# Performance work log

Hardware: AMD Instinct MI355X
Metric: run time of the kernel (lower is better)

## Reference

```python
import jax, jax.numpy as jnp
import numpy as np

B, H, W, C = 1, 64, 64, 256
HEADS, K, DIL = 8, 7, 2
HD = C // HEADS
FF = 4 * C
EPS = 1e-5
SCALE = 1.0 / float(np.sqrt(HD))


def _axis_indices(L, k, d):
    """NATTEN dilated neighborhood: per dilation-group clamped sliding window.
    Returns key indices [L,k] and relative-position-bias indices [L,k]."""
    i = np.arange(L)
    g, rem = i // d, i % d                      # position within dilation group
    lg = (L - rem + d - 1) // d                 # group length per position
    start = np.clip(g - k // 2, 0, lg - k)      # clamped window start (group coords)
    a = np.arange(k)
    kidx = (start[:, None] + a[None, :]) * d + rem[:, None]          # key coord
    bidx = start[:, None] + a[None, :] - g[:, None] + (k - 1)        # rpb coord in [0, 2k-2]
    return kidx.astype(np.int32), bidx.astype(np.int32)


def setup_inputs():
    key = jax.random.key(0)
    ks = jax.random.split(key, 8)
    p = lambda k_, sh: jax.random.normal(k_, sh, jnp.float32) * 0.02
    return {
        "x": jax.random.normal(ks[0], (B, H, W, C), jnp.float32),
        "ln1_g": jnp.ones((C,), jnp.float32), "ln1_b": jnp.zeros((C,), jnp.float32),
        "wq": p(ks[1], (C, C)), "bq": jnp.zeros((C,), jnp.float32),
        "wk": p(ks[2], (C, C)), "bk": jnp.zeros((C,), jnp.float32),
        "wv": p(ks[3], (C, C)), "bv": jnp.zeros((C,), jnp.float32),
        "rpb": p(ks[4], (HEADS, 2 * K - 1, 2 * K - 1)),
        "wo": p(ks[5], (C, C)), "bo": jnp.zeros((C,), jnp.float32),
        "ln2_g": jnp.ones((C,), jnp.float32), "ln2_b": jnp.zeros((C,), jnp.float32),
        "w1": p(ks[6], (C, FF)), "b1": jnp.zeros((FF,), jnp.float32),
        "w2": p(ks[7], (FF, C)), "b2": jnp.zeros((C,), jnp.float32),
    }


def _layer_norm(x, g, b):
    m = jnp.mean(x, -1, keepdims=True)
    v = jnp.mean(jnp.square(x - m), -1, keepdims=True)
    return (x - m) * jax.lax.rsqrt(v + EPS) * g + b


def reference(x, ln1_g, ln1_b, wq, bq, wk, bk, wv, bv, rpb, wo, bo,
              ln2_g, ln2_b, w1, b1, w2, b2):
    ih, bih = _axis_indices(H, K, DIL)   # [H,K]
    iw, biw = _axis_indices(W, K, DIL)   # [W,K]
    hs = _layer_norm(x, ln1_g, ln1_b)
    q = (hs @ wq + bq).reshape(B, H, W, HEADS, HD) * SCALE
    k = (hs @ wk + bk).reshape(B, H, W, HEADS, HD)
    v = (hs @ wv + bv).reshape(B, H, W, HEADS, HD)
    # gather dilated neighborhoods -> [B,H,W,K,K,heads,hd]
    k_nb = k[:, ih[:, None, :, None], iw[None, :, None, :], :, :]
    v_nb = v[:, ih[:, None, :, None], iw[None, :, None, :], :, :]
    # natten2dqkrpb: per-query scores over K*K dilated neighbors + rpb
    scores = jnp.einsum('bijnc,bijklnc->bnijkl', q, k_nb)
    bias = rpb[:, bih[:, None, :, None], biw[None, :, None, :]]  # [heads,H,W,K,K]
    scores = scores + bias[None]
    probs = jax.nn.softmax(scores.reshape(B, HEADS, H, W, K * K), axis=-1)
    # natten2dav
    ctx = jnp.einsum('bnijp,bijpnc->bijnc', probs,
                     v_nb.reshape(B, H, W, K * K, HEADS, HD))
    attn_out = ctx.reshape(B, H, W, C) @ wo + bo
    hs2 = x + attn_out                      # residual (layer_scale disabled: init 0.0)
    y = _layer_norm(hs2, ln2_g, ln2_b)
    y = jax.nn.gelu(y @ w1 + b1, approximate=False) @ w2 + b2
    return hs2 + y
```

## Files before the change

kernel.cpp:

```cpp
#include <hip/hip_runtime.h>
#include <math.h>

#define CC 256
#define NTOK 4096
#define NHEADS 8
#define HD 32
#define FFD 1024
#define LN_EPS 1e-5f
#define QSCALE 0.17677669529663687f

typedef __bf16 bf16x8 __attribute__((ext_vector_type(8)));
typedef float f32x4 __attribute__((ext_vector_type(4)));
typedef unsigned short u16x8 __attribute__((ext_vector_type(8)));

__device__ __forceinline__ unsigned short f2bf(float f) {
    unsigned u = __builtin_bit_cast(unsigned, f);
    u += 0x7fff + ((u >> 16) & 1);
    return (unsigned short)(u >> 16);
}
__device__ __forceinline__ float bf2f(unsigned short h) {
    unsigned u = ((unsigned)h) << 16;
    return __builtin_bit_cast(float, u);
}
__device__ __forceinline__ void gload16(const unsigned short* g, unsigned short* l) {
    __builtin_amdgcn_global_load_lds(
        (const __attribute__((address_space(1))) unsigned int*)(const void*)g,
        (__attribute__((address_space(3))) unsigned int*)(void*)l, 16, 0, 0);
}

__global__ void ln_kernel(const float* __restrict__ x, const float* __restrict__ g,
                          const float* __restrict__ b, unsigned short* __restrict__ out) {
    int wave = threadIdx.x >> 6;
    int lane = threadIdx.x & 63;
    int tok = blockIdx.x * 4 + wave;
    const float4 v = ((const float4*)(x + (size_t)tok * CC))[lane];
    float s  = v.x + v.y + v.z + v.w;
    float ss = v.x * v.x + v.y * v.y + v.z * v.z + v.w * v.w;
    #pragma unroll
    for (int o = 32; o > 0; o >>= 1) { s += __shfl_xor(s, o); ss += __shfl_xor(ss, o); }
    float m   = s * (1.0f / CC);
    float var = ss * (1.0f / CC) - m * m;
    float r   = rsqrtf(var + LN_EPS);
    float4 gv = ((const float4*)g)[lane];
    float4 bv = ((const float4*)b)[lane];
    ushort4 o4;
    o4.x = f2bf((v.x - m) * r * gv.x + bv.x);
    o4.y = f2bf((v.y - m) * r * gv.y + bv.y);
    o4.z = f2bf((v.z - m) * r * gv.z + bv.z);
    o4.w = f2bf((v.w - m) * r * gv.w + bv.w);
    ((ushort4*)(out + (size_t)tok * CC))[lane] = o4;
}

__global__ void setup_kernel(const float* __restrict__ wq, const float* __restrict__ wk,
                             const float* __restrict__ wv, const float* __restrict__ wo,
                             const float* __restrict__ w1, const float* __restrict__ w2,
                             const float* __restrict__ bq, const float* __restrict__ bk,
                             const float* __restrict__ bv,
                             unsigned short* __restrict__ wt_qkv, unsigned short* __restrict__ wo_t,
                             unsigned short* __restrict__ w1_t, unsigned short* __restrict__ w2_t,
                             float* __restrict__ bqkv) {
    int id = blockIdx.x;
    int t = threadIdx.x;
    if (id == 192) {
        bqkv[t]       = bq[t] * QSCALE;
        bqkv[256 + t] = bk[t];
        bqkv[512 + t] = bv[t];
        return;
    }
    const float* src; unsigned short* dst;
    int Kd, N, rowoff = 0, bx, by; float scale = 1.0f;
    if (id < 16)       { src = wq; dst = wt_qkv; Kd = 256;  N = 256;  scale = QSCALE; int l = id;       bx = l & 3;  by = l >> 2; }
    else if (id < 32)  { src = wk; dst = wt_qkv; Kd = 256;  N = 256;  rowoff = 256;   int l = id - 16;  bx = l & 3;  by = l >> 2; }
    else if (id < 48)  { src = wv; dst = wt_qkv; Kd = 256;  N = 256;  rowoff = 512;   int l = id - 32;  bx = l & 3;  by = l >> 2; }
    else if (id < 64)  { src = wo; dst = wo_t;   Kd = 256;  N = 256;                  int l = id - 48;  bx = l & 3;  by = l >> 2; }
    else if (id < 128) { src = w1; dst = w1_t;   Kd = 256;  N = 1024;                 int l = id - 64;  bx = l & 15; by = l >> 4; }
    else               { src = w2; dst = w2_t;   Kd = 1024; N = 256;                  int l = id - 128; bx = l & 3;  by = l >> 2; }
    int n0 = bx * 64, k0 = by * 64;
    __shared__ float tile[64][65];
    int cc = t & 63, rb = t >> 6;
    #pragma unroll
    for (int i = 0; i < 16; i++) {
        int r = rb + i * 4;
        tile[r][cc] = src[(size_t)(k0 + r) * N + n0 + cc];
    }
    __syncthreads();
    int n = t >> 2;
    #pragma unroll
    for (int i = 0; i < 8; i++) {
        int p = (t & 3) + i * 4;
        unsigned lo = f2bf(tile[2 * p][n] * scale);
        unsigned hi = f2bf(tile[2 * p + 1][n] * scale);
        *(unsigned*)(dst + (size_t)(rowoff + n0 + n) * Kd + k0 + 2 * p) = lo | (hi << 16);
    }
}

template<int BM, int BN, int KD, int ACT, bool ADD_RES, bool OUT_BF16>
__global__ __launch_bounds__(256) void mfma_gemm(
    const unsigned short* __restrict__ A, const unsigned short* __restrict__ Bt,
    const float* __restrict__ bias, const float* __restrict__ res,
    void* __restrict__ Cm, int N) {
    constexpr int WM = BM / 2, WN = BN / 2;
    constexpr int MF = WM / 16, NF = WN / 16;
    constexpr int NIT = KD / 32;
    __shared__ unsigned short lds[2][(BM + BN) * 32];
    const int t = threadIdx.x;
    const int lane = t & 63, w = t >> 6;
    const int wr = w >> 1, wc = w & 1;
    const int bm = blockIdx.y * BM, bn = blockIdx.x * BN;
    const int fr = lane & 15, sq = lane >> 4;
    const int aoff = (wr * WM + fr) * 64 + sq * 16;
    const int boff = (wc * WN + fr) * 64 + sq * 16;

    auto stage = [&](int it, int buf) {
        unsigned short* La = lds[buf];
        unsigned short* Lb = lds[buf] + BM * 32;
        if (BM * 4 == 256 || t < BM * 4)
            gload16(A + (size_t)(bm + (t >> 2)) * KD + it * 32 + (t & 3) * 8, La + t * 8);
        gload16(Bt + (size_t)(bn + (t >> 2)) * KD + it * 32 + (t & 3) * 8, Lb + t * 8);
    };

    f32x4 acc[MF][NF] = {};
    stage(0, 0);
    #pragma unroll
    for (int it = 0; it < NIT; ++it) {
        const int buf = it & 1;
        __syncthreads();
        if (it + 1 < NIT) stage(it + 1, buf ^ 1);
        const char* La = (const char*)lds[buf];
        const char* Lb = (const char*)(lds[buf] + BM * 32);
        bf16x8 af[MF], bfr[NF];
        #pragma unroll
        for (int i = 0; i < MF; i++) af[i] = *(const bf16x8*)(La + aoff + i * 1024);
        #pragma unroll
        for (int j = 0; j < NF; j++) bfr[j] = *(const bf16x8*)(Lb + boff + j * 1024);
        #pragma unroll
        for (int i = 0; i < MF; i++)
            #pragma unroll
            for (int j = 0; j < NF; j++)
                acc[i][j] = __builtin_amdgcn_mfma_f32_16x16x32_bf16(af[i], bfr[j], acc[i][j], 0, 0, 0);
    }
    #pragma unroll
    for (int i = 0; i < MF; i++) {
        int row0 = bm + wr * WM + i * 16 + sq * 4;
        #pragma unroll
        for (int j = 0; j < NF; j++) {
            int col = bn + wc * WN + j * 16 + fr;
            float bvv = bias[col];
            #pragma unroll
            for (int r = 0; r < 4; r++) {
                float v = acc[i][j][r] + bvv;
                if constexpr (ACT == 1) v = 0.5f * v * (1.0f + erff(v * 0.70710678118654752f));
                if constexpr (ADD_RES) v += res[(size_t)(row0 + r) * N + col];
                if constexpr (OUT_BF16)
                    ((unsigned short*)Cm)[(size_t)(row0 + r) * N + col] = f2bf(v);
                else
                    ((float*)Cm)[(size_t)(row0 + r) * N + col] = v;
            }
        }
    }
}

__global__ void attn_kernel(const unsigned short* __restrict__ qkv,
                            const float* __restrict__ rpb,
                            unsigned short* __restrict__ ctx) {
    __shared__ float ps[4][64];
    int wave = threadIdx.x >> 6;
    int lane = threadIdx.x & 63;
    int gid  = blockIdx.x * 4 + wave;
    int tok  = gid >> 3;
    int head = gid & 7;
    int i = tok >> 6, j = tok & 63;
    int gi = i >> 1, ri = i & 1;
    int gj = j >> 1, rj = j & 1;
    int si = min(max(gi - 3, 0), 25);
    int sj = min(max(gj - 3, 0), 25);

    float score = -1e30f;
    if (lane < 49) {
        int a1 = lane / 7, a2 = lane % 7;
        int kt = ((si + a1) * 2 + ri) * 64 + (sj + a2) * 2 + rj;
        const unsigned short* qp = qkv + (size_t)tok * 768 + head * HD;
        const unsigned short* kp = qkv + (size_t)kt * 768 + 256 + head * HD;
        float s = 0.0f;
        #pragma unroll
        for (int d = 0; d < HD; d += 8) {
            u16x8 qv8 = *(const u16x8*)(qp + d);
            u16x8 kv8 = *(const u16x8*)(kp + d);
            #pragma unroll
            for (int e = 0; e < 8; e++) s += bf2f(qv8[e]) * bf2f(kv8[e]);
        }
        score = s + rpb[(head * 13 + (si + a1 - gi + 6)) * 13 + (sj + a2 - gj + 6)];
    }
    float mx = score;
    #pragma unroll
    for (int o = 32; o > 0; o >>= 1) mx = fmaxf(mx, __shfl_xor(mx, o));
    float p = (lane < 49) ? __expf(score - mx) : 0.0f;
    float sum = p;
    #pragma unroll
    for (int o = 32; o > 0; o >>= 1) sum += __shfl_xor(sum, o);
    ps[wave][lane] = p / sum;

    int d = lane & 31, half = lane >> 5;
    const unsigned short* vb = qkv + 512 + head * HD + d;
    float acc = 0.0f;
    #pragma unroll
    for (int s = 0; s < 25; ++s) {
        int nb = 2 * s + half;
        if (nb < 49) {
            int a1 = nb / 7, a2 = nb % 7;
            int kt = ((si + a1) * 2 + ri) * 64 + (sj + a2) * 2 + rj;
            acc += ps[wave][nb] * bf2f(vb[(size_t)kt * 768]);
        }
    }
    acc += __shfl_xor(acc, 32);
    if (lane < HD)
        ctx[(size_t)tok * CC + head * HD + lane] = f2bf(acc);
}

extern "C" void kernel_launch(void* const* d_in, const int* in_sizes, int n_in,
                              void* d_out, int out_size, void* d_ws, size_t ws_size,
                              hipStream_t stream) {
    const float* x     = (const float*)d_in[0];
    const float* ln1_g = (const float*)d_in[1];
    const float* ln1_b = (const float*)d_in[2];
    const float* wq    = (const float*)d_in[3];
    const float* bq    = (const float*)d_in[4];
    const float* wk    = (const float*)d_in[5];
    const float* bk    = (const float*)d_in[6];
    const float* wv    = (const float*)d_in[7];
    const float* bv    = (const float*)d_in[8];
    const float* rpb   = (const float*)d_in[9];
    const float* wo    = (const float*)d_in[10];
    const float* bo    = (const float*)d_in[11];
    const float* ln2_g = (const float*)d_in[12];
    const float* ln2_b = (const float*)d_in[13];
    const float* w1    = (const float*)d_in[14];
    const float* b1    = (const float*)d_in[15];
    const float* w2    = (const float*)d_in[16];
    const float* b2    = (const float*)d_in[17];

    char* wsb = (char*)d_ws;
    unsigned short* hs_bf  = (unsigned short*)(wsb);
    unsigned short* qkv_bf = (unsigned short*)(wsb + (2u << 20));
    unsigned short* ctx_bf = (unsigned short*)(wsb + (8u << 20));
    float*          hs2    = (float*)(wsb + (10u << 20));
    unsigned short* y1_bf  = (unsigned short*)(wsb + (14u << 20));
    unsigned short* gm_bf  = (unsigned short*)(wsb + (16u << 20));
    unsigned short* wt_qkv = (unsigned short*)(wsb + (24u << 20));
    unsigned short* wo_t   = wt_qkv + 768 * 256;
    unsigned short* w1_t   = wo_t + 256 * 256;
    unsigned short* w2_t   = w1_t + 1024 * 256;
    float*          bqkv   = (float*)(w2_t + 256 * 1024);

    setup_kernel<<<193, 256, 0, stream>>>(wq, wk, wv, wo, w1, w2, bq, bk, bv,
                                          wt_qkv, wo_t, w1_t, w2_t, bqkv);
    ln_kernel<<<NTOK / 4, 256, 0, stream>>>(x, ln1_g, ln1_b, hs_bf);
    mfma_gemm<64, 64, 256, 0, false, true><<<dim3(12, 64), 256, 0, stream>>>(
        hs_bf, wt_qkv, bqkv, nullptr, qkv_bf, 768);
    attn_kernel<<<NTOK * NHEADS / 4, 256, 0, stream>>>(qkv_bf, rpb, ctx_bf);
    mfma_gemm<32, 64, 256, 0, true, false><<<dim3(4, 128), 256, 0, stream>>>(
        ctx_bf, wo_t, bo, x, hs2, 256);
    ln_kernel<<<NTOK / 4, 256, 0, stream>>>(hs2, ln2_g, ln2_b, y1_bf);
    mfma_gemm<64, 64, 256, 1, false, true><<<dim3(16, 64), 256, 0, stream>>>(
        y1_bf, w1_t, b1, nullptr, gm_bf, 1024);
    mfma_gemm<32, 64, 1024, 0, true, false><<<dim3(4, 128), 256, 0, stream>>>(
        gm_bf, w2_t, b2, hs2, (float*)d_out, 256);
}
```

Before: 164.7 us.

## Load full K into LDS for K=256 GEMMs, deepen pipeline stages, restructure attention per token

The K=256 GEMMs now load the whole A and B K-slab into LDS with a single barrier instead of a double-buffered loop of 32-wide steps. The K=1024 GEMM now uses 64-wide double-buffered stages, which halves the number of barriers. The attention kernel now runs one wave per token covering all 8 heads, with 8 lanes per head. Each lane handles 4 channels and reduces with shuffles, so the query and neighbour K/V rows are read as contiguous 512-byte segments instead of many scattered per-lane loads. Full-K staging uses more LDS per block (up to 64 KB), which may lower occupancy.

```diff
diff --git a/kernel.cpp b/kernel.cpp
--- a/kernel.cpp
+++ b/kernel.cpp
@@ -11,7 +11,6 @@
 
 typedef __bf16 bf16x8 __attribute__((ext_vector_type(8)));
 typedef float f32x4 __attribute__((ext_vector_type(4)));
-typedef unsigned short u16x8 __attribute__((ext_vector_type(8)));
 
 __device__ __forceinline__ unsigned short f2bf(float f) {
     unsigned u = __builtin_bit_cast(unsigned, f);
@@ -94,45 +93,48 @@
     }
 }
 
-template<int BM, int BN, int KD, int ACT, bool ADD_RES, bool OUT_BF16>
-__global__ __launch_bounds__(256) void mfma_gemm(
+template<int BM, int BN, int ACT, bool ADD_RES, bool OUT_BF16>
+__global__ __launch_bounds__(256) void gemm_res(
     const unsigned short* __restrict__ A, const unsigned short* __restrict__ Bt,
     const float* __restrict__ bias, const float* __restrict__ res,
     void* __restrict__ Cm, int N) {
+    constexpr int KD = 256;
     constexpr int WM = BM / 2, WN = BN / 2;
     constexpr int MF = WM / 16, NF = WN / 16;
-    constexpr int NIT = KD / 32;
-    __shared__ unsigned short lds[2][(BM + BN) * 32];
+    __shared__ unsigned short lds[(BM + BN) * KD];
+    unsigned short* Bl = lds + BM * KD;
     const int t = threadIdx.x;
     const int lane = t & 63, w = t >> 6;
     const int wr = w >> 1, wc = w & 1;
     const int bm = blockIdx.y * BM, bn = blockIdx.x * BN;
     const int fr = lane & 15, sq = lane >> 4;
-    const int aoff = (wr * WM + fr) * 64 + sq * 16;
-    const int boff = (wc * WN + fr) * 64 + sq * 16;
-
-    auto stage = [&](int it, int buf) {
-        unsigned short* La = lds[buf];
-        unsigned short* Lb = lds[buf] + BM * 32;
-        if (BM * 4 == 256 || t < BM * 4)
-            gload16(A + (size_t)(bm + (t >> 2)) * KD + it * 32 + (t & 3) * 8, La + t * 8);
-        gload16(Bt + (size_t)(bn + (t >> 2)) * KD + it * 32 + (t & 3) * 8, Lb + t * 8);
-    };
+
+    #pragma unroll
+    for (int i = 0; i < BM * 32 / 256; i++) {
+        int c = t + i * 256;
+        int kk = c / (BM * 4), r = (c % (BM * 4)) >> 2, jj = c & 3;
+        gload16(A + (size_t)(bm + r) * KD + kk * 32 + jj * 8, lds + c * 8);
+    }
+    #pragma unroll
+    for (int i = 0; i < BN * 32 / 256; i++) {
+        int c = t + i * 256;
+        int kk = c / (BN * 4), r = (c % (BN * 4)) >> 2, jj = c & 3;
+        gload16(Bt + (size_t)(bn + r) * KD + kk * 32 + jj * 8, Bl + c * 8);
+    }
+    __syncthreads();
 
     f32x4 acc[MF][NF] = {};
-    stage(0, 0);
-    #pragma unroll
-    for (int it = 0; it < NIT; ++it) {
-        const int buf = it & 1;
-        __syncthreads();
-        if (it + 1 < NIT) stage(it + 1, buf ^ 1);
-        const char* La = (const char*)lds[buf];
-        const char* Lb = (const char*)(lds[buf] + BM * 32);
+    #pragma unroll
+    for (int kk = 0; kk < 8; kk++) {
+        const char* La = (const char*)lds + kk * BM * 64;
+        const char* Lb = (const char*)Bl  + kk * BN * 64;
         bf16x8 af[MF], bfr[NF];
         #pragma unroll
-        for (int i = 0; i < MF; i++) af[i] = *(const bf16x8*)(La + aoff + i * 1024);
-        #pragma unroll
-        for (int j = 0; j < NF; j++) bfr[j] = *(const bf16x8*)(Lb + boff + j * 1024);
+        for (int i = 0; i < MF; i++)
+            af[i] = *(const bf16x8*)(La + (wr * WM + i * 16 + fr) * 64 + sq * 16);
+        #pragma unroll
+        for (int j = 0; j < NF; j++)
+            bfr[j] = *(const bf16x8*)(Lb + (wc * WN + j * 16 + fr) * 64 + sq * 16);
         #pragma unroll
         for (int i = 0; i < MF; i++)
             #pragma unroll
@@ -160,61 +162,146 @@
     }
 }
 
-__global__ void attn_kernel(const unsigned short* __restrict__ qkv,
-                            const float* __restrict__ rpb,
-                            unsigned short* __restrict__ ctx) {
-    __shared__ float ps[4][64];
+template<int BM, int BN, int KD, int ACT, bool ADD_RES, bool OUT_BF16>
+__global__ __launch_bounds__(256) void gemm_db(
+    const unsigned short* __restrict__ A, const unsigned short* __restrict__ Bt,
+    const float* __restrict__ bias, const float* __restrict__ res,
+    void* __restrict__ Cm, int N) {
+    constexpr int WM = BM / 2, WN = BN / 2;
+    constexpr int MF = WM / 16, NF = WN / 16;
+    constexpr int NIT = KD / 64;
+    __shared__ unsigned short lds[2][(BM + BN) * 64];
+    const int t = threadIdx.x;
+    const int lane = t & 63, w = t >> 6;
+    const int wr = w >> 1, wc = w & 1;
+    const int bm = blockIdx.y * BM, bn = blockIdx.x * BN;
+    const int fr = lane & 15, sq = lane >> 4;
+
+    auto stage = [&](int it, int buf) {
+        unsigned short* La = lds[buf];
+        unsigned short* Lb = lds[buf] + BM * 64;
+        #pragma unroll
+        for (int i = 0; i < BM * 8 / 256; i++) {
+            int c = t + i * 256;
+            int kk = c / (BM * 4), r = (c % (BM * 4)) >> 2, jj = c & 3;
+            gload16(A + (size_t)(bm + r) * KD + it * 64 + kk * 32 + jj * 8, La + c * 8);
+        }
+        #pragma unroll
+        for (int i = 0; i < BN * 8 / 256; i++) {
+            int c = t + i * 256;
+            int kk = c / (BN * 4), r = (c % (BN * 4)) >> 2, jj = c & 3;
+            gload16(Bt + (size_t)(bn + r) * KD + it * 64 + kk * 32 + jj * 8, Lb + c * 8);
+        }
+    };
+
+    f32x4 acc[MF][NF] = {};
+    stage(0, 0);
+    for (int it = 0; it < NIT; ++it) {
+        const int buf = it & 1;
+        __syncthreads();
+        if (it + 1 < NIT) stage(it + 1, buf ^ 1);
+        #pragma unroll
+        for (int kk = 0; kk < 2; kk++) {
+            const char* La = (const char*)(lds[buf]) + kk * BM * 64;
+            const char* Lb = (const char*)(lds[buf] + BM * 64) + kk * BN * 64;
+            bf16x8 af[MF], bfr[NF];
+            #pragma unroll
+            for (int i = 0; i < MF; i++)
+                af[i] = *(const bf16x8*)(La + (wr * WM + i * 16 + fr) * 64 + sq * 16);
+            #pragma unroll
+            for (int j = 0; j < NF; j++)
+                bfr[j] = *(const bf16x8*)(Lb + (wc * WN + j * 16 + fr) * 64 + sq * 16);
+            #pragma unroll
+            for (int i = 0; i < MF; i++)
+                #pragma unroll
+                for (int j = 0; j < NF; j++)
+                    acc[i][j] = __builtin_amdgcn_mfma_f32_16x16x32_bf16(af[i], bfr[j], acc[i][j], 0, 0, 0);
+        }
+    }
+    #pragma unroll
+    for (int i = 0; i < MF; i++) {
+        int row0 = bm + wr * WM + i * 16 + sq * 4;
+        #pragma unroll
+        for (int j = 0; j < NF; j++) {
+            int col = bn + wc * WN + j * 16 + fr;
+            float bvv = bias[col];
+            #pragma unroll
+            for (int r = 0; r < 4; r++) {
+                float v = acc[i][j][r] + bvv;
+                if constexpr (ACT == 1) v = 0.5f * v * (1.0f + erff(v * 0.70710678118654752f));
+                if constexpr (ADD_RES) v += res[(size_t)(row0 + r) * N + col];
+                if constexpr (OUT_BF16)
+                    ((unsigned short*)Cm)[(size_t)(row0 + r) * N + col] = f2bf(v);
+                else
+                    ((float*)Cm)[(size_t)(row0 + r) * N + col] = v;
+            }
+        }
+    }
+}
+
+__global__ __launch_bounds__(256) void attn_kernel(
+    const unsigned short* __restrict__ qkv, const float* __restrict__ rpb,
+    unsigned short* __restrict__ ctx) {
     int wave = threadIdx.x >> 6;
     int lane = threadIdx.x & 63;
-    int gid  = blockIdx.x * 4 + wave;
-    int tok  = gid >> 3;
-    int head = gid & 7;
+    int tok  = blockIdx.x * 4 + wave;
     int i = tok >> 6, j = tok & 63;
     int gi = i >> 1, ri = i & 1;
     int gj = j >> 1, rj = j & 1;
     int si = min(max(gi - 3, 0), 25);
     int sj = min(max(gj - 3, 0), 25);
-
-    float score = -1e30f;
-    if (lane < 49) {
-        int a1 = lane / 7, a2 = lane % 7;
-        int kt = ((si + a1) * 2 + ri) * 64 + (sj + a2) * 2 + rj;
-        const unsigned short* qp = qkv + (size_t)tok * 768 + head * HD;
-        const unsigned short* kp = qkv + (size_t)kt * 768 + 256 + head * HD;
-        float s = 0.0f;
-        #pragma unroll
-        for (int d = 0; d < HD; d += 8) {
-            u16x8 qv8 = *(const u16x8*)(qp + d);
-            u16x8 kv8 = *(const u16x8*)(kp + d);
-            #pragma unroll
-            for (int e = 0; e < 8; e++) s += bf2f(qv8[e]) * bf2f(kv8[e]);
-        }
-        score = s + rpb[(head * 13 + (si + a1 - gi + 6)) * 13 + (sj + a2 - gj + 6)];
-    }
-    float mx = score;
-    #pragma unroll
-    for (int o = 32; o > 0; o >>= 1) mx = fmaxf(mx, __shfl_xor(mx, o));
-    float p = (lane < 49) ? __expf(score - mx) : 0.0f;
-    float sum = p;
-    #pragma unroll
-    for (int o = 32; o > 0; o >>= 1) sum += __shfl_xor(sum, o);
-    ps[wave][lane] = p / sum;
-
-    int d = lane & 31, half = lane >> 5;
-    const unsigned short* vb = qkv + 512 + head * HD + d;
-    float acc = 0.0f;
-    #pragma unroll
-    for (int s = 0; s < 25; ++s) {
-        int nb = 2 * s + half;
-        if (nb < 49) {
-            int a1 = nb / 7, a2 = nb % 7;
-            int kt = ((si + a1) * 2 + ri) * 64 + (sj + a2) * 2 + rj;
-            acc += ps[wave][nb] * bf2f(vb[(size_t)kt * 768]);
-        }
-    }
-    acc += __shfl_xor(acc, 32);
-    if (lane < HD)
-        ctx[(size_t)tok * CC + head * HD + lane] = f2bf(acc);
+    int h = lane >> 3, e = lane & 7;
+
+    ushort4 qv = *(const ushort4*)(qkv + (size_t)tok * 768 + (lane << 2));
+    float q0 = bf2f(qv.x), q1 = bf2f(qv.y), q2 = bf2f(qv.z), q3 = bf2f(qv.w);
+
+    int krow[7], jcol[7];
+    #pragma unroll
+    for (int a = 0; a < 7; a++) {
+        krow[a] = ((si + a) * 2 + ri) * 64;
+        jcol[a] = (sj + a) * 2 + rj;
+    }
+    const float* rb = rpb + h * 169 + (si - gi + 6) * 13 + (sj - gj + 6);
+
+    float sc[7];
+    #pragma unroll
+    for (int t2 = 0; t2 < 7; t2++) sc[t2] = -1e30f;
+
+    #pragma unroll
+    for (int n = 0; n < 49; n++) {
+        int kt = krow[n / 7] + jcol[n % 7];
+        const ushort4 kv = *(const ushort4*)(qkv + (size_t)kt * 768 + 256 + (lane << 2));
+        float s = q0 * bf2f(kv.x) + q1 * bf2f(kv.y) + q2 * bf2f(kv.z) + q3 * bf2f(kv.w);
+        s += __shfl_xor(s, 1); s += __shfl_xor(s, 2); s += __shfl_xor(s, 4);
+        s += rb[(n / 7) * 13 + (n % 7)];
+        if (e == (n & 7)) sc[n >> 3] = s;
+    }
+    float mx = sc[0];
+    #pragma unroll
+    for (int t2 = 1; t2 < 7; t2++) mx = fmaxf(mx, sc[t2]);
+    mx = fmaxf(mx, __shfl_xor(mx, 1));
+    mx = fmaxf(mx, __shfl_xor(mx, 2));
+    mx = fmaxf(mx, __shfl_xor(mx, 4));
+    float pr[7], sum = 0.0f;
+    #pragma unroll
+    for (int t2 = 0; t2 < 7; t2++) { pr[t2] = __expf(sc[t2] - mx); sum += pr[t2]; }
+    sum += __shfl_xor(sum, 1); sum += __shfl_xor(sum, 2); sum += __shfl_xor(sum, 4);
+    float inv = 1.0f / sum;
+    #pragma unroll
+    for (int t2 = 0; t2 < 7; t2++) pr[t2] *= inv;
+
+    float a0 = 0.0f, a1 = 0.0f, a2 = 0.0f, a3 = 0.0f;
+    #pragma unroll
+    for (int n = 0; n < 49; n++) {
+        int kt = krow[n / 7] + jcol[n % 7];
+        float p = __shfl(pr[n >> 3], n & 7, 8);
+        const ushort4 vv = *(const ushort4*)(qkv + (size_t)kt * 768 + 512 + (lane << 2));
+        a0 += p * bf2f(vv.x); a1 += p * bf2f(vv.y);
+        a2 += p * bf2f(vv.z); a3 += p * bf2f(vv.w);
+    }
+    ushort4 o;
+    o.x = f2bf(a0); o.y = f2bf(a1); o.z = f2bf(a2); o.w = f2bf(a3);
+    ((ushort4*)(ctx + (size_t)tok * 256))[lane] = o;
 }
 
 extern "C" void kernel_launch(void* const* d_in, const int* in_sizes, int n_in,
@@ -255,14 +342,14 @@
     setup_kernel<<<193, 256, 0, stream>>>(wq, wk, wv, wo, w1, w2, bq, bk, bv,
                                           wt_qkv, wo_t, w1_t, w2_t, bqkv);
     ln_kernel<<<NTOK / 4, 256, 0, stream>>>(x, ln1_g, ln1_b, hs_bf);
-    mfma_gemm<64, 64, 256, 0, false, true><<<dim3(12, 64), 256, 0, stream>>>(
+    gemm_res<64, 64, 0, false, true><<<dim3(12, 64), 256, 0, stream>>>(
         hs_bf, wt_qkv, bqkv, nullptr, qkv_bf, 768);
-    attn_kernel<<<NTOK * NHEADS / 4, 256, 0, stream>>>(qkv_bf, rpb, ctx_bf);
-    mfma_gemm<32, 64, 256, 0, true, false><<<dim3(4, 128), 256, 0, stream>>>(
+    attn_kernel<<<NTOK / 4, 256, 0, stream>>>(qkv_bf, rpb, ctx_bf);
+    gemm_res<32, 64, 0, true, false><<<dim3(4, 128), 256, 0, stream>>>(
         ctx_bf, wo_t, bo, x, hs2, 256);
     ln_kernel<<<NTOK / 4, 256, 0, stream>>>(hs2, ln2_g, ln2_b, y1_bf);
-    mfma_gemm<64, 64, 256, 1, false, true><<<dim3(16, 64), 256, 0, stream>>>(
+    gemm_res<64, 64, 1, false, true><<<dim3(16, 64), 256, 0, stream>>>(
         y1_bf, w1_t, b1, nullptr, gm_bf, 1024);
-    mfma_gemm<32, 64, 1024, 0, true, false><<<dim3(4, 128), 256, 0, stream>>>(
+    gemm_db<32, 64, 1024, 0, true, false><<<dim3(4, 128), 256, 0, stream>>>(
         gm_bf, w2_t, b2, hs2, (float*)d_out, 256);
 }
```

New measurement: 176.5 us. 1.07x slower.
